# Optimization experiments

Hardware: AMD Instinct MI355X
Metric: run time of the kernel (lower is better)

## Reference

```python
import jax, jax.numpy as jnp
from jax import lax
import numpy as np

C = 56; DI = 112; DS = 16; R = 4; K = 4; NB = 10; UP = 3
B, H, W = 1, 64, 64

def conv2d(x, w, b=None, pad=1, groups=1):
    out = lax.conv_general_dilated(x, w, (1, 1), [(pad, pad), (pad, pad)],
                                   feature_group_count=groups,
                                   dimension_numbers=('NCHW', 'OIHW', 'NCHW'))
    if b is not None:
        out = out + b[None, :, None, None]
    return out

def ln_last(x, w, b, eps=1e-5):
    mu = x.mean(-1, keepdims=True)
    var = ((x - mu) ** 2).mean(-1, keepdims=True)
    return (x - mu) / jnp.sqrt(var + eps) * w + b

def ln_cf(x, w, b, eps=1e-6):
    mu = x.mean(1, keepdims=True)
    var = ((x - mu) ** 2).mean(1, keepdims=True)
    return (x - mu) / jnp.sqrt(var + eps) * w[None, :, None, None] + b[None, :, None, None]

def bsconv(x, pw_w, dw_w, dw_b):
    x = conv2d(x, pw_w, pad=0)
    return conv2d(x, dw_w, dw_b, pad=1, groups=dw_w.shape[0])

def ss2d(x, p):
    # x: (B,H,W,C) -> SS2D (VMamba 4-direction selective scan)
    b, h, w, _ = x.shape
    L = h * w
    xz = x @ p['inproj_w'].T                        # (B,H,W,2*DI)
    xin, z = jnp.split(xz, 2, axis=-1)
    xc = jnp.transpose(xin, (0, 3, 1, 2))           # (B,DI,H,W)
    xc = jax.nn.silu(conv2d(xc, p['conv_w'], p['conv_b'], pad=1, groups=DI))
    xf = xc.reshape(b, DI, L)
    xt = jnp.swapaxes(xc, 2, 3).reshape(b, DI, L)
    x_hwwh = jnp.stack([xf, xt], axis=1)            # (B,2,DI,L)
    xs = jnp.concatenate([x_hwwh, jnp.flip(x_hwwh, -1)], axis=1)  # (B,K,DI,L)
    x_dbl = jnp.einsum('bkdl,kcd->bkcl', xs, p['xproj_w'])
    dts, Bs, Cs = jnp.split(x_dbl, [R, R + DS], axis=2)
    dts = jnp.einsum('bkrl,kdr->bkdl', dts, p['dt_w'])
    A = -jnp.exp(p['Alog'].reshape(K, DI, DS))
    delta = jax.nn.softplus(dts + p['dt_b'][None, :, :, None])    # (B,K,DI,L)

    def step(hst, inp):
        dl, xl, bl, cl = inp
        dA = jnp.exp(dl[..., None] * A[None])       # (B,K,DI,DS)
        hst = dA * hst + (dl * xl)[..., None] * bl[:, :, None, :]
        y = jnp.einsum('bkdn,bkn->bkd', hst, cl)
        return hst, y

    seq = (jnp.transpose(delta, (3, 0, 1, 2)), jnp.transpose(xs, (3, 0, 1, 2)),
           jnp.transpose(Bs, (3, 0, 1, 2)), jnp.transpose(Cs, (3, 0, 1, 2)))
    h0 = jnp.zeros((b, K, DI, DS), x.dtype)
    _, ys = lax.scan(step, h0, seq)                 # (L,B,K,DI)
    out_y = jnp.transpose(ys, (1, 2, 3, 0)) + p['D'].reshape(K, DI)[None, :, :, None] * xs
    inv = jnp.flip(out_y[:, 2:4], -1)
    y1 = out_y[:, 0]
    y2 = inv[:, 0]
    y3 = jnp.swapaxes(inv[:, 1].reshape(b, DI, w, h), 2, 3).reshape(b, DI, L)
    y4 = jnp.swapaxes(out_y[:, 1].reshape(b, DI, w, h), 2, 3).reshape(b, DI, L)
    y = jnp.swapaxes(y1 + y2 + y3 + y4, 1, 2).reshape(b, h, w, DI)
    y = ln_last(y, p['onorm_w'], p['onorm_b'])
    y = y * jax.nn.silu(z)
    return y @ p['outproj_w'].T

def safm(x, mfr_w, mfr_b, aggr_w, aggr_b):
    b, c, h, w = x.shape
    ch = c // 4
    parts = jnp.split(x, 4, axis=1)
    outs = []
    for i in range(4):
        s = parts[i]
        f = 2 ** i
        if i > 0:
            s = s.reshape(b, ch, h // f, f, w // f, f).max(axis=(3, 5))
        s = conv2d(s, mfr_w[i], mfr_b[i], pad=1, groups=ch)
        if i > 0:
            s = jnp.repeat(jnp.repeat(s, f, axis=2), f, axis=3)
        outs.append(s)
    out = conv2d(jnp.concatenate(outs, axis=1), aggr_w, aggr_b, pad=0)
    return jax.nn.gelu(out, approximate=False) * x

def afd(x, p):
    xn = jnp.transpose(x, (0, 2, 3, 1))
    xn = xn + ss2d(ln_last(xn, p['ln1_w'], p['ln1_b']), p)   # VSSBlock residual
    x = jnp.transpose(xn, (0, 3, 1, 2))
    x = x + safm(ln_cf(x, p['norm_w'], p['norm_b']), p['mfr_w'], p['mfr_b'], p['aggr_w'], p['aggr_b'])
    return x, x

def _forward(x, fea_pw_w, fea_dw_w, fea_dw_b,
             blk_ln1_w, blk_ln1_b, blk_inproj_w, blk_conv_w, blk_conv_b,
             blk_xproj_w, blk_dt_w, blk_dt_b, blk_Alog, blk_D,
             blk_onorm_w, blk_onorm_b, blk_outproj_w,
             blk_norm_w, blk_norm_b, blk_mfr_w, blk_mfr_b, blk_aggr_w, blk_aggr_b,
             c1_w, c1_b, norm_w, norm_b, c2_pw_w, c2_dw_w, c2_dw_b, up_w, up_b):
    out_fea = bsconv(x, fea_pw_w, fea_dw_w, fea_dw_b)
    bp = {'ln1_w': blk_ln1_w, 'ln1_b': blk_ln1_b, 'inproj_w': blk_inproj_w,
          'conv_w': blk_conv_w, 'conv_b': blk_conv_b, 'xproj_w': blk_xproj_w,
          'dt_w': blk_dt_w, 'dt_b': blk_dt_b, 'Alog': blk_Alog, 'D': blk_D,
          'onorm_w': blk_onorm_w, 'onorm_b': blk_onorm_b, 'outproj_w': blk_outproj_w,
          'norm_w': blk_norm_w, 'norm_b': blk_norm_b, 'mfr_w': blk_mfr_w,
          'mfr_b': blk_mfr_b, 'aggr_w': blk_aggr_w, 'aggr_b': blk_aggr_b}
    _, outs = lax.scan(afd, out_fea, bp)            # (NB,B,C,H,W) in B1..B10 order
    b, _, h, w = out_fea.shape
    trunk = jnp.transpose(outs, (1, 0, 2, 3, 4)).reshape(b, NB * C, h, w)
    out_B = conv2d(trunk, c1_w, c1_b, pad=0)
    out_B = jax.nn.gelu(ln_cf(out_B, norm_w, norm_b), approximate=False)
    out_lr = bsconv(out_B, c2_pw_w, c2_dw_w, c2_dw_b) + out_fea
    up = conv2d(out_lr, up_w, up_b, pad=1)          # (B, 3*UP*UP, H, W)
    oc = up.shape[1] // (UP * UP)
    ps = up.reshape(b, oc, UP, UP, h, w)
    return jnp.transpose(ps, (0, 1, 4, 2, 5, 3)).reshape(b, oc, h * UP, w * UP)

def setup_inputs():
    key = jax.random.key(0)
    ks = iter(jax.random.split(key, 40))
    rn = lambda shape, s=0.05: jax.random.normal(next(ks), shape, jnp.float32) * s
    ones = lambda shape: jnp.ones(shape, jnp.float32)
    zeros = lambda shape: jnp.zeros(shape, jnp.float32)
    return {
        'x': jax.random.normal(next(ks), (B, 3, H, W), jnp.float32),
        'fea_pw_w': rn((C, 3, 1, 1), 0.3),
        'fea_dw_w': rn((C, 1, 3, 3), 0.3),
        'fea_dw_b': zeros((C,)),
        'blk_ln1_w': ones((NB, C)), 'blk_ln1_b': zeros((NB, C)),
        'blk_inproj_w': rn((NB, 2 * DI, C)),
        'blk_conv_w': rn((NB, DI, 1, 3, 3), 0.2), 'blk_conv_b': zeros((NB, DI)),
        'blk_xproj_w': rn((NB, K, R + 2 * DS, DI)),
        'blk_dt_w': rn((NB, K, DI, R), 0.2),
        'blk_dt_b': jnp.full((NB, K, DI), -4.6, jnp.float32),
        'blk_Alog': jnp.broadcast_to(jnp.log(jnp.arange(1, DS + 1, dtype=jnp.float32)), (NB, K * DI, DS)) + jnp.zeros((NB, K * DI, DS), jnp.float32),
        'blk_D': ones((NB, K * DI)),
        'blk_onorm_w': ones((NB, DI)), 'blk_onorm_b': zeros((NB, DI)),
        'blk_outproj_w': rn((NB, C, DI)),
        'blk_norm_w': ones((NB, C)), 'blk_norm_b': zeros((NB, C)),
        'blk_mfr_w': rn((NB, 4, C // 4, 1, 3, 3), 0.2), 'blk_mfr_b': zeros((NB, 4, C // 4)),
        'blk_aggr_w': rn((NB, C, C, 1, 1)), 'blk_aggr_b': zeros((NB, C)),
        'c1_w': rn((C, NB * C, 1, 1)), 'c1_b': zeros((C,)),
        'norm_w': ones((C,)), 'norm_b': zeros((C,)),
        'c2_pw_w': rn((C, C, 1, 1)), 'c2_dw_w': rn((C, 1, 3, 3), 0.2), 'c2_dw_b': zeros((C,)),
        'up_w': rn((3 * UP * UP, C, 3, 3)), 'up_b': zeros((3 * UP * UP,)),
    }

def reference(x, fea_pw_w, fea_dw_w, fea_dw_b,
              blk_ln1_w, blk_ln1_b, blk_inproj_w, blk_conv_w, blk_conv_b,
              blk_xproj_w, blk_dt_w, blk_dt_b, blk_Alog, blk_D,
              blk_onorm_w, blk_onorm_b, blk_outproj_w,
              blk_norm_w, blk_norm_b, blk_mfr_w, blk_mfr_b, blk_aggr_w, blk_aggr_b,
              c1_w, c1_b, norm_w, norm_b, c2_pw_w, c2_dw_w, c2_dw_b, up_w, up_b):
    return _forward(x, fea_pw_w, fea_dw_w, fea_dw_b,
                    blk_ln1_w, blk_ln1_b, blk_inproj_w, blk_conv_w, blk_conv_b,
                    blk_xproj_w, blk_dt_w, blk_dt_b, blk_Alog, blk_D,
                    blk_onorm_w, blk_onorm_b, blk_outproj_w,
                    blk_norm_w, blk_norm_b, blk_mfr_w, blk_mfr_b, blk_aggr_w, blk_aggr_b,
                    c1_w, c1_b, norm_w, norm_b, c2_pw_w, c2_dw_w, c2_dw_b, up_w, up_b)
```

## Files before the change

kernel.cpp:

```cpp
#include <hip/hip_runtime.h>
#include <hip/hip_bf16.h>

#define HW 64
#define L4 4096
#define CC 56
#define DI 112
#define DSN 16
#define NBLK 10

typedef const float* BP;

__device__ __forceinline__ float bf(BP p, int i) { return p[i]; }
__device__ __forceinline__ float siluf(float x) { return x / (1.f + __expf(-x)); }
__device__ __forceinline__ float geluf(float x) { return 0.5f * x * (1.f + erff(x * 0.70710678f)); }

__global__ void k_fea_pw(BP x, BP w, float* __restrict__ t0) {
    int tid = blockIdx.x * blockDim.x + threadIdx.x;
    if (tid >= CC * L4) return;
    int c = tid >> 12, l = tid & 4095;
    float acc = 0.f;
    for (int i = 0; i < 3; ++i) acc += bf(x, i * L4 + l) * bf(w, c * 3 + i);
    t0[tid] = acc;
}

__global__ void __launch_bounds__(256) k_dw3x3t(
        const float* __restrict__ src, BP w, BP bvec, float* __restrict__ dst,
        int act, const float* __restrict__ addsrc) {
    int c = blockIdx.x >> 4;
    int tile = blockIdx.x & 15;
    int y0 = (tile >> 2) * 16, x0 = (tile & 3) * 16;
    __shared__ float sT[18 * 18];
    const float* sc = src + (size_t)c * L4;
    for (int idx = threadIdx.x; idx < 324; idx += 256) {
        int iy = idx / 18, ix = idx - iy * 18;
        int gy = y0 - 1 + iy, gx = x0 - 1 + ix;
        sT[idx] = (gy >= 0 && gy < 64 && gx >= 0 && gx < 64) ? sc[gy * 64 + gx] : 0.f;
    }
    __syncthreads();
    int py = threadIdx.x >> 4, px = threadIdx.x & 15;
    BP wr = w + c * 9;
    float acc = bvec ? bvec[c] : 0.f;
    #pragma unroll
    for (int ky = 0; ky < 3; ++ky)
        #pragma unroll
        for (int kx = 0; kx < 3; ++kx)
            acc += sT[(py + ky) * 18 + px + kx] * wr[ky * 3 + kx];
    if (act) acc = siluf(acc);
    int l = (y0 + py) * 64 + x0 + px;
    if (addsrc) acc += addsrc[(size_t)c * L4 + l];
    dst[(size_t)c * L4 + l] = acc;
}

__global__ void __launch_bounds__(256) k_ln56(
        const float* __restrict__ src, BP w, BP b, float* __restrict__ dst,
        float eps, int gelu_after) {
    int lane = threadIdx.x & 63;
    int cg = threadIdx.x >> 6;
    int l0 = blockIdx.x * 64;
    __shared__ float sS[56 * 64];
    __shared__ float sPa[4][64], sPb[4][64];
    __shared__ float sMu[64], sRs[64];
    float ps = 0.f, ps2 = 0.f;
    for (int c = cg * 14; c < cg * 14 + 14; ++c) {
        float v = src[(size_t)c * L4 + l0 + lane];
        sS[c * 64 + lane] = v; ps += v; ps2 += v * v;
    }
    sPa[cg][lane] = ps; sPb[cg][lane] = ps2;
    __syncthreads();
    if (threadIdx.x < 64) {
        float s = sPa[0][lane] + sPa[1][lane] + sPa[2][lane] + sPa[3][lane];
        float s2 = sPb[0][lane] + sPb[1][lane] + sPb[2][lane] + sPb[3][lane];
        float mu = s / 56.f;
        float var = fmaxf(s2 / 56.f - mu * mu, 0.f);
        sMu[lane] = mu; sRs[lane] = rsqrtf(var + eps);
    }
    __syncthreads();
    float mu = sMu[lane], rs = sRs[lane];
    for (int c = cg * 14; c < cg * 14 + 14; ++c) {
        float v = (sS[c * 64 + lane] - mu) * rs * w[c] + b[c];
        if (gelu_after) v = geluf(v);
        dst[(size_t)c * L4 + l0 + lane] = v;
    }
}

__global__ void __launch_bounds__(256) k_gemm(
        const float* __restrict__ src, BP w, BP bvec, const float* __restrict__ addsrc,
        float* __restrict__ dst, int nin, int nout) {
    int lane = threadIdx.x & 63;
    int jg = threadIdx.x >> 6;
    int l0 = blockIdx.x * 64;
    int j0 = blockIdx.y * 16;
    __shared__ __align__(16) float sS[56 * 64];
    __shared__ __align__(16) float sw[16 * 56];
    float acc[4] = {0.f, 0.f, 0.f, 0.f};

    for (int i0 = 0; i0 < nin; i0 += 56) {
        __syncthreads();
        for (int idx = threadIdx.x; idx < 56 * 64; idx += 256) {
            int ii = idx >> 6, px = idx & 63;
            sS[idx] = src[(size_t)(i0 + ii) * L4 + l0 + px];
        }
        for (int idx = threadIdx.x; idx < 16 * 56; idx += 256) {
            int jj = idx / 56, ii = idx - jj * 56;
            int j = j0 + jj;
            sw[idx] = (j < nout) ? w[(size_t)j * nin + i0 + ii] : 0.f;
        }
        __syncthreads();
        #pragma unroll
        for (int ii = 0; ii < 56; ii += 4) {
            float s0 = sS[(ii + 0) * 64 + lane];
            float s1 = sS[(ii + 1) * 64 + lane];
            float s2 = sS[(ii + 2) * 64 + lane];
            float s3 = sS[(ii + 3) * 64 + lane];
            #pragma unroll
            for (int jj = 0; jj < 4; ++jj) {
                const float4 wv = *(const float4*)&sw[(jg * 4 + jj) * 56 + ii];
                acc[jj] += s0 * wv.x + s1 * wv.y + s2 * wv.z + s3 * wv.w;
            }
        }
    }
    int l = l0 + lane;
    #pragma unroll
    for (int jj = 0; jj < 4; ++jj) {
        int j = j0 + jg * 4 + jj;
        if (j >= nout) continue;
        float v = acc[jj];
        if (bvec) v += bf(bvec, j);
        size_t idx = (size_t)j * L4 + l;
        if (addsrc) v += addsrc[idx];
        dst[idx] = v;
    }
}

__global__ void __launch_bounds__(256) k_xproj(
        const float* __restrict__ src, BP w, float* __restrict__ dst) {
    int lane = threadIdx.x & 31;
    int jg = threadIdx.x >> 5;
    int l0 = blockIdx.x * 32;
    int j0 = blockIdx.y * 16;
    __shared__ __align__(16) float sS[112 * 32];
    __shared__ __align__(16) float sw[16 * 112];
    float acc[2] = {0.f, 0.f};

    for (int idx = threadIdx.x; idx < 112 * 32; idx += 256) {
        int ii = idx >> 5, px = idx & 31;
        sS[idx] = src[(size_t)ii * L4 + l0 + px];
    }
    for (int idx = threadIdx.x; idx < 16 * 112; idx += 256) {
        int jj = idx / 112, ii = idx - jj * 112;
        sw[idx] = w[(size_t)(j0 + jj) * 112 + ii];
    }
    __syncthreads();
    #pragma unroll
    for (int ii = 0; ii < 112; ii += 4) {
        float s0 = sS[(ii + 0) * 32 + lane];
        float s1 = sS[(ii + 1) * 32 + lane];
        float s2 = sS[(ii + 2) * 32 + lane];
        float s3 = sS[(ii + 3) * 32 + lane];
        #pragma unroll
        for (int jj = 0; jj < 2; ++jj) {
            const float4 wv = *(const float4*)&sw[(jg * 2 + jj) * 112 + ii];
            acc[jj] += s0 * wv.x + s1 * wv.y + s2 * wv.z + s3 * wv.w;
        }
    }
    __syncthreads();
    #pragma unroll
    for (int jj = 0; jj < 2; ++jj)
        sS[(jg * 2 + jj) * 32 + lane] = acc[jj];
    __syncthreads();
    for (int idx = threadIdx.x; idx < 16 * 32; idx += 256) {
        int cidx = idx & 15, l2 = idx >> 4;
        int j = j0 + cidx;
        int k = j / 36, c = j - k * 36;
        dst[((size_t)k * L4 + l0 + l2) * 36 + c] = sS[cidx * 32 + l2];
    }
}

__global__ void __launch_bounds__(256) k_gemm_ln(
        const float* __restrict__ src, BP lnw, BP lnb, BP w,
        float* __restrict__ dst, int nout) {
    int lane = threadIdx.x & 63;
    int jg = threadIdx.x >> 6;
    int l0 = blockIdx.x * 64;
    int j0 = blockIdx.y * 16;
    __shared__ __align__(16) float sS[56 * 64];
    __shared__ __align__(16) float sw[16 * 56];
    __shared__ float sLw[56], sLb[56];
    float acc[4] = {0.f, 0.f, 0.f, 0.f};

    for (int idx = threadIdx.x; idx < 56 * 64; idx += 256) {
        int ii = idx >> 6, px = idx & 63;
        sS[idx] = src[(size_t)ii * L4 + l0 + px];
    }
    for (int idx = threadIdx.x; idx < 16 * 56; idx += 256) {
        int jj = idx / 56, ii = idx - jj * 56;
        int j = j0 + jj;
        sw[idx] = (j < nout) ? w[(size_t)j * 56 + ii] : 0.f;
    }
    if (threadIdx.x < 56) { sLw[threadIdx.x] = lnw[threadIdx.x]; sLb[threadIdx.x] = lnb[threadIdx.x]; }
    __syncthreads();
    if (threadIdx.x < 64) {
        int px = threadIdx.x;
        float s = 0.f, s2 = 0.f;
        for (int ii = 0; ii < 56; ++ii) { float v = sS[ii * 64 + px]; s += v; s2 += v * v; }
        float mu = s / 56.f;
        float var = fmaxf(s2 / 56.f - mu * mu, 0.f);
        float rstd = rsqrtf(var + 1e-5f);
        for (int ii = 0; ii < 56; ++ii)
            sS[ii * 64 + px] = (sS[ii * 64 + px] - mu) * rstd * sLw[ii] + sLb[ii];
    }
    __syncthreads();
    #pragma unroll
    for (int ii = 0; ii < 56; ii += 4) {
        float s0 = sS[(ii + 0) * 64 + lane];
        float s1 = sS[(ii + 1) * 64 + lane];
        float s2 = sS[(ii + 2) * 64 + lane];
        float s3 = sS[(ii + 3) * 64 + lane];
        #pragma unroll
        for (int jj = 0; jj < 4; ++jj) {
            const float4 wv = *(const float4*)&sw[(jg * 4 + jj) * 56 + ii];
            acc[jj] += s0 * wv.x + s1 * wv.y + s2 * wv.z + s3 * wv.w;
        }
    }
    int l = l0 + lane;
    #pragma unroll
    for (int jj = 0; jj < 4; ++jj) {
        int j = j0 + jg * 4 + jj;
        if (j < nout) dst[(size_t)j * L4 + l] = acc[jj];
    }
}

#define SPAD(p) ((p) + ((p) >> 5))
__global__ void __launch_bounds__(1024) k_scan(
        const float* __restrict__ xc, const float* __restrict__ pk,
        BP Alog, BP dtw, BP dtb, float* __restrict__ ybuf) {
    int pair = blockIdx.x;
    int n = threadIdx.x & 15;
    int c = threadIdx.x >> 4;
    int k = pair / DI, d = pair - k * DI;
    float a = -__expf(Alog[pair * DSN + n]);
    float w0 = dtw[pair * 4 + 0], w1 = dtw[pair * 4 + 1];
    float w2 = dtw[pair * 4 + 2], w3 = dtw[pair * 4 + 3];
    float db = dtb[pair];
    const float* xptr = xc + (size_t)d * L4;
    const float* pkk = pk + (size_t)k * L4 * 36;
    float* yptr = ybuf + (size_t)pair * L4;

    __shared__ float sDl[4224];
    __shared__ float sDlx[4224];
    __shared__ float sP[64 * 16];
    __shared__ float sHe[64 * 16];
    __shared__ float sCar[64 * 16];

    for (int p = threadIdx.x; p < L4; p += 1024) {
        const float* row = pkk + (size_t)p * 36;
        float v = db + row[0] * w0 + row[1] * w1 + row[2] * w2 + row[3] * w3;
        float dl = fmaxf(v, 0.f) + __logf(1.f + __expf(-fabsf(v)));
        sDl[SPAD(p)] = dl;
        sDlx[SPAD(p)] = dl * xptr[p];
    }
    __syncthreads();

    int p0, dp;
    if (k == 0)      { p0 = c * 64;        dp = 1;   }
    else if (k == 1) { p0 = c;             dp = 64;  }
    else if (k == 2) { p0 = 4095 - c * 64; dp = -1;  }
    else             { p0 = 4095 - c;      dp = -64; }
    long rstep = (long)dp * 36;

    float h = 0.f, P = 1.f;
    {
        int p = p0;
        const float* rB = pkk + (size_t)p0 * 36 + 4 + n;
        #pragma unroll 4
        for (int j = 0; j < 64; ++j) {
            int q = SPAD(p);
            float e = __expf(sDl[q] * a);
            h = e * h + sDlx[q] * (*rB);
            P *= e;
            p += dp; rB += rstep;
        }
    }
    sP[c * 16 + n] = P;
    sHe[c * 16 + n] = h;
    __syncthreads();

    if (threadIdx.x < 16) {
        float H = 0.f;
        for (int cc = 0; cc < 64; ++cc) {
            sCar[cc * 16 + n] = H;
            H = sP[cc * 16 + n] * H + sHe[cc * 16 + n];
        }
    }
    __syncthreads();

    h = sCar[c * 16 + n];
    {
        int p = p0;
        const float* rB = pkk + (size_t)p0 * 36 + 4 + n;
        const float* rC = pkk + (size_t)p0 * 36 + 20 + n;
        #pragma unroll 4
        for (int j = 0; j < 64; ++j) {
            int q = SPAD(p);
            float e = __expf(sDl[q] * a);
            h = e * h + sDlx[q] * (*rB);
            float y = h * (*rC);
            y += __shfl_xor(y, 1, 16);
            y += __shfl_xor(y, 2, 16);
            y += __shfl_xor(y, 4, 16);
            y += __shfl_xor(y, 8, 16);
            if (n == 0) yptr[p] = y;
            p += dp; rB += rstep; rC += rstep;
        }
    }
}

__global__ void __launch_bounds__(256) k_comb_proj(
        const float* __restrict__ ybuf, const float* __restrict__ xc,
        const float* __restrict__ zbuf, BP Dp, BP ow, BP ob, BP opw,
        const float* __restrict__ xin, BP nw, BP nbv,
        float* __restrict__ x_mid, float* __restrict__ xln) {
    int lane = threadIdx.x & 63;
    int cg = threadIdx.x >> 6;
    int l0 = blockIdx.x * 64;
    __shared__ __align__(16) float sY[112 * 64];
    __shared__ __align__(16) float sW[56 * 112];
    __shared__ float sPa[4][64], sPb[4][64];
    __shared__ float sMu[64], sRs[64];

    float ps = 0.f, ps2 = 0.f;
    for (int d = cg * 28; d < cg * 28 + 28; ++d) {
        float Ds = Dp[d] + Dp[DI + d] + Dp[2 * DI + d] + Dp[3 * DI + d];
        float v = ybuf[(size_t)d * L4 + l0 + lane]
                + ybuf[(size_t)(DI + d) * L4 + l0 + lane]
                + ybuf[(size_t)(2 * DI + d) * L4 + l0 + lane]
                + ybuf[(size_t)(3 * DI + d) * L4 + l0 + lane]
                + Ds * xc[(size_t)d * L4 + l0 + lane];
        sY[d * 64 + lane] = v; ps += v; ps2 += v * v;
    }
    sPa[cg][lane] = ps; sPb[cg][lane] = ps2;
    for (int idx = threadIdx.x; idx < 56 * 112; idx += 256) sW[idx] = opw[idx];
    __syncthreads();
    if (threadIdx.x < 64) {
        float s = sPa[0][lane] + sPa[1][lane] + sPa[2][lane] + sPa[3][lane];
        float s2 = sPb[0][lane] + sPb[1][lane] + sPb[2][lane] + sPb[3][lane];
        float mu = s / 112.f;
        float var = fmaxf(s2 / 112.f - mu * mu, 0.f);
        sMu[lane] = mu; sRs[lane] = rsqrtf(var + 1e-5f);
    }
    __syncthreads();
    {
        float mu = sMu[lane], rs = sRs[lane];
        for (int d = cg * 28; d < cg * 28 + 28; ++d) {
            float v = (sY[d * 64 + lane] - mu) * rs * ow[d] + ob[d];
            float z = zbuf[(size_t)d * L4 + l0 + lane];
            sY[d * 64 + lane] = v * siluf(z);
        }
    }
    __syncthreads();

    float acc[14];
    #pragma unroll
    for (int jj = 0; jj < 14; ++jj) acc[jj] = 0.f;
    #pragma unroll 2
    for (int ii = 0; ii < 112; ii += 4) {
        float s0 = sY[(ii + 0) * 64 + lane];
        float s1 = sY[(ii + 1) * 64 + lane];
        float s2 = sY[(ii + 2) * 64 + lane];
        float s3 = sY[(ii + 3) * 64 + lane];
        #pragma unroll
        for (int jj = 0; jj < 14; ++jj) {
            const float4 wv = *(const float4*)&sW[(cg * 14 + jj) * 112 + ii];
            acc[jj] += s0 * wv.x + s1 * wv.y + s2 * wv.z + s3 * wv.w;
        }
    }
    int l = l0 + lane;
    float ps3 = 0.f, ps4 = 0.f;
    #pragma unroll
    for (int jj = 0; jj < 14; ++jj) {
        int j = cg * 14 + jj;
        float v = acc[jj] + xin[(size_t)j * L4 + l];
        acc[jj] = v;
        x_mid[(size_t)j * L4 + l] = v;
        ps3 += v; ps4 += v * v;
    }
    __syncthreads();
    sPa[cg][lane] = ps3; sPb[cg][lane] = ps4;
    __syncthreads();
    if (threadIdx.x < 64) {
        float s = sPa[0][lane] + sPa[1][lane] + sPa[2][lane] + sPa[3][lane];
        float s2 = sPb[0][lane] + sPb[1][lane] + sPb[2][lane] + sPb[3][lane];
        float mu = s / 56.f;
        float var = fmaxf(s2 / 56.f - mu * mu, 0.f);
        sMu[lane] = mu; sRs[lane] = rsqrtf(var + 1e-6f);
    }
    __syncthreads();
    {
        float mu = sMu[lane], rs = sRs[lane];
        #pragma unroll
        for (int jj = 0; jj < 14; ++jj) {
            int j = cg * 14 + jj;
            xln[(size_t)j * L4 + l] = (acc[jj] - mu) * rs * nw[j] + nbv[j];
        }
    }
}

__global__ void __launch_bounds__(256) k_safm(
        const float* __restrict__ xln, BP mw, BP mb,
        float* __restrict__ s0, float* __restrict__ s1,
        float* __restrict__ s2, float* __restrict__ s3) {
    int b = blockIdx.x;
    if (b < 224) {
        int c = b >> 4;
        int tile = b & 15;
        int y0 = (tile >> 2) * 16, x0 = (tile & 3) * 16;
        __shared__ float sT[18 * 18];
        const float* sc = xln + (size_t)c * L4;
        for (int idx = threadIdx.x; idx < 324; idx += 256) {
            int iy = idx / 18, ix = idx - iy * 18;
            int gy = y0 - 1 + iy, gx = x0 - 1 + ix;
            sT[idx] = (gy >= 0 && gy < 64 && gx >= 0 && gx < 64) ? sc[gy * 64 + gx] : 0.f;
        }
        __syncthreads();
        int py = threadIdx.x >> 4, px = threadIdx.x & 15;
        BP wr = mw + c * 9;
        float acc = mb[c];
        #pragma unroll
        for (int ky = 0; ky < 3; ++ky)
            #pragma unroll
            for (int kx = 0; kx < 3; ++kx)
                acc += sT[(py + ky) * 18 + px + kx] * wr[ky * 3 + kx];
        s0[c * L4 + (y0 + py) * 64 + x0 + px] = acc;
    } else {
        int bb = b - 224;
        int i = bb / 14 + 1;
        int c = bb % 14;
        int S = 64 >> i;
        int f = 1 << i;
        __shared__ float sP[34 * 34];
        int W2 = S + 2;
        for (int idx = threadIdx.x; idx < W2 * W2; idx += 256) sP[idx] = 0.f;
        __syncthreads();
        const float* sc = xln + (size_t)(i * 14 + c) * L4;
        for (int cell = threadIdx.x; cell < S * S; cell += 256) {
            int y = cell / S, x = cell - y * S;
            float m = -3.4e38f;
            for (int dy = 0; dy < f; ++dy)
                for (int dx = 0; dx < f; ++dx)
                    m = fmaxf(m, sc[(y * f + dy) * 64 + x * f + dx]);
            sP[(y + 1) * W2 + x + 1] = m;
        }
        __syncthreads();
        BP wr = mw + (i * 14 + c) * 9;
        float bias = mb[i * 14 + c];
        float* dst = (i == 1) ? s1 : (i == 2) ? s2 : s3;
        for (int cell = threadIdx.x; cell < S * S; cell += 256) {
            int y = cell / S, x = cell - y * S;
            float acc = bias;
            #pragma unroll
            for (int ky = 0; ky < 3; ++ky)
                #pragma unroll
                for (int kx = 0; kx < 3; ++kx)
                    acc += sP[(y + ky) * W2 + x + kx] * wr[ky * 3 + kx];
            dst[c * S * S + cell] = acc;
        }
    }
}

__global__ void k_aggr(const float* __restrict__ s0, const float* __restrict__ s1,
                       const float* __restrict__ s2, const float* __restrict__ s3,
                       const float* __restrict__ xln, const float* __restrict__ x_mid,
                       BP aw, BP ab, float* __restrict__ out) {
    int tid = blockIdx.x * blockDim.x + threadIdx.x;
    if (tid >= CC * L4) return;
    int c = tid >> 12, l = tid & 4095;
    int h = l >> 6, w = l & 63;
    int o1 = (h >> 1) * 32 + (w >> 1);
    int o2 = (h >> 2) * 16 + (w >> 2);
    int o3 = (h >> 3) * 8 + (w >> 3);
    float acc = bf(ab, c);
    BP wr = aw + c * 56;
    for (int cg = 0; cg < 14; ++cg) acc += s0[cg * 4096 + l]  * bf(wr, cg);
    for (int cg = 0; cg < 14; ++cg) acc += s1[cg * 1024 + o1] * bf(wr, 14 + cg);
    for (int cg = 0; cg < 14; ++cg) acc += s2[cg * 256 + o2]  * bf(wr, 28 + cg);
    for (int cg = 0; cg < 14; ++cg) acc += s3[cg * 64 + o3]   * bf(wr, 42 + cg);
    out[tid] = x_mid[tid] + geluf(acc) * xln[tid];
}

__global__ void __launch_bounds__(256) k_up(
        const float* __restrict__ out_lr, BP uw, BP ub, float* __restrict__ out) {
    __shared__ float sIn[56 * 36];
    __shared__ float sW[27 * 56 * 9];
    int b = blockIdx.x;
    int y0 = (b >> 4) * 4, x0 = (b & 15) * 4;
    for (int idx = threadIdx.x; idx < 56 * 36; idx += 256) {
        int cc = idx / 36; int rem = idx - cc * 36; int iy = rem / 6, ix = rem - iy * 6;
        int gy = y0 - 1 + iy, gx = x0 - 1 + ix;
        sIn[idx] = (gy >= 0 && gy < 64 && gx >= 0 && gx < 64)
                 ? out_lr[(size_t)cc * L4 + gy * 64 + gx] : 0.f;
    }
    for (int idx = threadIdx.x; idx < 27 * 56 * 9; idx += 256) sW[idx] = uw[idx];
    __syncthreads();
    int px = threadIdx.x & 15;
    int og = threadIdx.x >> 4;
    int dy = px >> 2, dx = px & 3;
    for (int oo = 0; oo < 2; ++oo) {
        int o = og * 2 + oo;
        if (o >= 27) break;
        float acc = ub[o];
        const float* wb = &sW[o * 504];
        for (int cc = 0; cc < 56; ++cc) {
            const float* ib = &sIn[cc * 36 + dy * 6 + dx];
            const float* wc = wb + cc * 9;
            acc += ib[0] * wc[0] + ib[1] * wc[1] + ib[2] * wc[2]
                 + ib[6] * wc[3] + ib[7] * wc[4] + ib[8] * wc[5]
                 + ib[12] * wc[6] + ib[13] * wc[7] + ib[14] * wc[8];
        }
        int h = y0 + dy, wv = x0 + dx;
        int ch = o / 9, rr = (o % 9) / 3, ss = o % 3;
        out[ch * 36864 + (h * 3 + rr) * 192 + (wv * 3 + ss)] = acc;
    }
}

extern "C" void kernel_launch(void* const* d_in, const int* in_sizes, int n_in,
                              void* d_out, int out_size, void* d_ws, size_t ws_size,
                              hipStream_t stream) {
    BP in0  = (BP)d_in[0];
    BP in1  = (BP)d_in[1];
    BP in2  = (BP)d_in[2];
    BP in3  = (BP)d_in[3];
    BP in4  = (BP)d_in[4];
    BP in5  = (BP)d_in[5];
    BP in6  = (BP)d_in[6];
    BP in7  = (BP)d_in[7];
    BP in8  = (BP)d_in[8];
    BP in9  = (BP)d_in[9];
    BP in10 = (BP)d_in[10];
    BP in11 = (BP)d_in[11];
    BP in12 = (BP)d_in[12];
    BP in13 = (BP)d_in[13];
    BP in14 = (BP)d_in[14];
    BP in15 = (BP)d_in[15];
    BP in16 = (BP)d_in[16];
    BP in17 = (BP)d_in[17];
    BP in18 = (BP)d_in[18];
    BP in19 = (BP)d_in[19];
    BP in20 = (BP)d_in[20];
    BP in21 = (BP)d_in[21];
    BP in22 = (BP)d_in[22];
    BP in23 = (BP)d_in[23];
    BP in24 = (BP)d_in[24];
    BP in25 = (BP)d_in[25];
    BP in26 = (BP)d_in[26];
    BP in27 = (BP)d_in[27];
    BP in28 = (BP)d_in[28];
    BP in29 = (BP)d_in[29];
    BP in30 = (BP)d_in[30];
    BP in31 = (BP)d_in[31];

    float* ws = (float*)d_ws;
    float* trunk   = ws; ws += 560 * L4;
    float* out_fea = ws; ws += CC * L4;
    float* t0      = ws; ws += CC * L4;
    float* xz      = ws; ws += 224 * L4;
    float* xc      = ws; ws += DI * L4;
    float* pk      = ws; ws += 4 * 36 * L4;
    float* ybuf    = ws; ws += 4 * DI * L4;
    float* x_mid   = ws; ws += CC * L4;
    float* xln     = ws; ws += CC * L4;
    float* s0      = ws; ws += 14 * 4096;
    float* s1      = ws; ws += 14 * 1024;
    float* s2      = ws; ws += 14 * 256;
    float* s3      = ws; ws += 14 * 64;
    float* bufB    = ws; ws += CC * L4;
    float* gB      = ws; ws += CC * L4;
    float* tbuf    = ws; ws += CC * L4;
    float* out_lr  = ws; ws += CC * L4;

    auto nb256 = [](int n) { return dim3((n + 255) / 256); };
    auto gemm_grid = [](int nout) { return dim3(64, (nout + 15) / 16); };

    k_fea_pw<<<nb256(CC * L4), 256, 0, stream>>>(in0, in1, t0);
    k_dw3x3t<<<dim3(CC * 16), 256, 0, stream>>>(t0, in2, in3, out_fea, 0, nullptr);

    for (int nb = 0; nb < NBLK; ++nb) {
        const float* xin = (nb == 0) ? out_fea : trunk + (size_t)(nb - 1) * CC * L4;
        float* xout = trunk + (size_t)nb * CC * L4;
        BP ln1w = in4 + nb * 56,        ln1b = in5 + nb * 56;
        BP ipw  = in6 + nb * 224 * 56;
        BP cw   = in7 + nb * 112 * 9,   cb   = in8 + nb * 112;
        BP xpw  = in9 + nb * 4 * 36 * 112;
        BP dtw  = in10 + nb * 4 * 112 * 4, dtb = in11 + nb * 448;
        BP alog = in12 + nb * 448 * 16, Dp   = in13 + nb * 448;
        BP onw  = in14 + nb * 112,      onb  = in15 + nb * 112;
        BP opw  = in16 + nb * 56 * 112;
        BP nw   = in17 + nb * 56,       nbv  = in18 + nb * 56;
        BP mw   = in19 + nb * 4 * 14 * 9, mb = in20 + nb * 56;
        BP aw   = in21 + nb * 56 * 56,  ab   = in22 + nb * 56;

        k_gemm_ln<<<gemm_grid(224), 256, 0, stream>>>(xin, ln1w, ln1b, ipw, xz, 224);
        k_dw3x3t<<<dim3(DI * 16), 256, 0, stream>>>(xz, cw, cb, xc, 1, nullptr);
        k_xproj<<<dim3(128, 9), 256, 0, stream>>>(xc, xpw, pk);
        k_scan<<<dim3(4 * DI), 1024, 0, stream>>>(xc, pk, alog, dtw, dtb, ybuf);
        k_comb_proj<<<dim3(64), 256, 0, stream>>>(ybuf, xc, xz + 112 * L4, Dp, onw, onb, opw,
                                                  xin, nw, nbv, x_mid, xln);
        k_safm<<<dim3(266), 256, 0, stream>>>(xln, mw, mb, s0, s1, s2, s3);
        k_aggr<<<nb256(CC * L4), 256, 0, stream>>>(s0, s1, s2, s3, xln, x_mid, aw, ab, xout);
    }

    k_gemm<<<gemm_grid(56), 256, 0, stream>>>(trunk, in23, in24, nullptr, bufB, 560, 56);
    k_ln56<<<dim3(64), 256, 0, stream>>>(bufB, in25, in26, gB, 1e-6f, 1);
    k_gemm<<<gemm_grid(56), 256, 0, stream>>>(gB, in27, nullptr, nullptr, tbuf, 56, 56);
    k_dw3x3t<<<dim3(CC * 16), 256, 0, stream>>>(tbuf, in28, in29, out_lr, 0, out_fea);
    k_up<<<dim3(256), 256, 0, stream>>>(out_lr, in30, in31, (float*)d_out);
}
```

Baseline: 1.407 ms.

## Split-K the final 1x1 conv, parallelize scan carry, and shrink comb_proj tiles

The final 560-input 1x1 conv is split along K into 5 slices, each writing partial sums. A new LN kernel adds the partials and the bias before normalizing and applying GELU. The serial 64-step carry propagation in the scan kernel becomes a log-step Hillis-Steele prefix over chunks. k_comb_proj moves from 64 blocks of 64 pixels to 256 blocks of 16 pixels to raise occupancy. In exchange, the partials cost extra memory traffic, the prefix scan adds more block syncs, and each comb_proj block now reloads the full weight matrix.

```diff
diff --git a/kernel.cpp b/kernel.cpp
--- a/kernel.cpp
+++ b/kernel.cpp
@@ -51,9 +51,8 @@
     dst[(size_t)c * L4 + l] = acc;
 }
 
-__global__ void __launch_bounds__(256) k_ln56(
-        const float* __restrict__ src, BP w, BP b, float* __restrict__ dst,
-        float eps, int gelu_after) {
+__global__ void __launch_bounds__(256) k_ln56g(
+        const float* __restrict__ part, BP bias, BP w, BP b, float* __restrict__ dst) {
     int lane = threadIdx.x & 63;
     int cg = threadIdx.x >> 6;
     int l0 = blockIdx.x * 64;
@@ -62,7 +61,10 @@
     __shared__ float sMu[64], sRs[64];
     float ps = 0.f, ps2 = 0.f;
     for (int c = cg * 14; c < cg * 14 + 14; ++c) {
-        float v = src[(size_t)c * L4 + l0 + lane];
+        float v = bias[c];
+        #pragma unroll
+        for (int z = 0; z < 5; ++z)
+            v += part[(size_t)(z * 56 + c) * L4 + l0 + lane];
         sS[c * 64 + lane] = v; ps += v; ps2 += v * v;
     }
     sPa[cg][lane] = ps; sPb[cg][lane] = ps2;
@@ -72,14 +74,13 @@
         float s2 = sPb[0][lane] + sPb[1][lane] + sPb[2][lane] + sPb[3][lane];
         float mu = s / 56.f;
         float var = fmaxf(s2 / 56.f - mu * mu, 0.f);
-        sMu[lane] = mu; sRs[lane] = rsqrtf(var + eps);
+        sMu[lane] = mu; sRs[lane] = rsqrtf(var + 1e-6f);
     }
     __syncthreads();
     float mu = sMu[lane], rs = sRs[lane];
     for (int c = cg * 14; c < cg * 14 + 14; ++c) {
         float v = (sS[c * 64 + lane] - mu) * rs * w[c] + b[c];
-        if (gelu_after) v = geluf(v);
-        dst[(size_t)c * L4 + l0 + lane] = v;
+        dst[(size_t)c * L4 + l0 + lane] = geluf(v);
     }
 }
 
@@ -129,6 +130,50 @@
         size_t idx = (size_t)j * L4 + l;
         if (addsrc) v += addsrc[idx];
         dst[idx] = v;
+    }
+}
+
+__global__ void __launch_bounds__(256) k_c1(
+        const float* __restrict__ src, BP w, float* __restrict__ part) {
+    int lane = threadIdx.x & 63;
+    int jg = threadIdx.x >> 6;
+    int l0 = blockIdx.x * 64;
+    int j0 = blockIdx.y * 16;
+    int z = blockIdx.z;
+    __shared__ __align__(16) float sS[56 * 64];
+    __shared__ __align__(16) float sw[16 * 56];
+    float acc[4] = {0.f, 0.f, 0.f, 0.f};
+
+    for (int i0 = z * 112; i0 < z * 112 + 112; i0 += 56) {
+        __syncthreads();
+        for (int idx = threadIdx.x; idx < 56 * 64; idx += 256) {
+            int ii = idx >> 6, px = idx & 63;
+            sS[idx] = src[(size_t)(i0 + ii) * L4 + l0 + px];
+        }
+        for (int idx = threadIdx.x; idx < 16 * 56; idx += 256) {
+            int jj = idx / 56, ii = idx - jj * 56;
+            int j = j0 + jj;
+            sw[idx] = (j < 56) ? w[(size_t)j * 560 + i0 + ii] : 0.f;
+        }
+        __syncthreads();
+        #pragma unroll
+        for (int ii = 0; ii < 56; ii += 4) {
+            float s0 = sS[(ii + 0) * 64 + lane];
+            float s1 = sS[(ii + 1) * 64 + lane];
+            float s2 = sS[(ii + 2) * 64 + lane];
+            float s3 = sS[(ii + 3) * 64 + lane];
+            #pragma unroll
+            for (int jj = 0; jj < 4; ++jj) {
+                const float4 wv = *(const float4*)&sw[(jg * 4 + jj) * 56 + ii];
+                acc[jj] += s0 * wv.x + s1 * wv.y + s2 * wv.z + s3 * wv.w;
+            }
+        }
+    }
+    int l = l0 + lane;
+    #pragma unroll
+    for (int jj = 0; jj < 4; ++jj) {
+        int j = j0 + jg * 4 + jj;
+        if (j < 56) part[(size_t)(z * 56 + j) * L4 + l] = acc[jj];
     }
 }
 
@@ -250,7 +295,6 @@
     __shared__ float sDlx[4224];
     __shared__ float sP[64 * 16];
     __shared__ float sHe[64 * 16];
-    __shared__ float sCar[64 * 16];
 
     for (int p = threadIdx.x; p < L4; p += 1024) {
         const float* row = pkk + (size_t)p * 36;
@@ -281,20 +325,21 @@
             p += dp; rB += rstep;
         }
     }
-    sP[c * 16 + n] = P;
-    sHe[c * 16 + n] = h;
-    __syncthreads();
-
-    if (threadIdx.x < 16) {
-        float H = 0.f;
-        for (int cc = 0; cc < 64; ++cc) {
-            sCar[cc * 16 + n] = H;
-            H = sP[cc * 16 + n] * H + sHe[cc * 16 + n];
-        }
-    }
-    __syncthreads();
-
-    h = sCar[c * 16 + n];
+    int idx = c * 16 + n;
+    sP[idx] = P;
+    sHe[idx] = h;
+    __syncthreads();
+
+    for (int off = 1; off < 64; off <<= 1) {
+        float pC = sP[idx], hC = sHe[idx];
+        float pL = 0.f, hL = 0.f;
+        if (c >= off) { pL = sP[idx - off * 16]; hL = sHe[idx - off * 16]; }
+        __syncthreads();
+        if (c >= off) { sP[idx] = pC * pL; sHe[idx] = pC * hL + hC; }
+        __syncthreads();
+    }
+
+    h = (c > 0) ? sHe[idx - 16] : 0.f;
     {
         int p = p0;
         const float* rB = pkk + (size_t)p0 * 36 + 4 + n;
@@ -320,30 +365,30 @@
         const float* __restrict__ zbuf, BP Dp, BP ow, BP ob, BP opw,
         const float* __restrict__ xin, BP nw, BP nbv,
         float* __restrict__ x_mid, float* __restrict__ xln) {
-    int lane = threadIdx.x & 63;
-    int cg = threadIdx.x >> 6;
-    int l0 = blockIdx.x * 64;
-    __shared__ __align__(16) float sY[112 * 64];
+    int lane = threadIdx.x & 15;
+    int grp = threadIdx.x >> 4;
+    int l0 = blockIdx.x * 16;
+    __shared__ __align__(16) float sY[112 * 16];
     __shared__ __align__(16) float sW[56 * 112];
-    __shared__ float sPa[4][64], sPb[4][64];
-    __shared__ float sMu[64], sRs[64];
+    __shared__ float sPa[16][16], sPb[16][16];
+    __shared__ float sMu[16], sRs[16];
 
     float ps = 0.f, ps2 = 0.f;
-    for (int d = cg * 28; d < cg * 28 + 28; ++d) {
+    for (int d = grp * 7; d < grp * 7 + 7; ++d) {
         float Ds = Dp[d] + Dp[DI + d] + Dp[2 * DI + d] + Dp[3 * DI + d];
         float v = ybuf[(size_t)d * L4 + l0 + lane]
                 + ybuf[(size_t)(DI + d) * L4 + l0 + lane]
                 + ybuf[(size_t)(2 * DI + d) * L4 + l0 + lane]
                 + ybuf[(size_t)(3 * DI + d) * L4 + l0 + lane]
                 + Ds * xc[(size_t)d * L4 + l0 + lane];
-        sY[d * 64 + lane] = v; ps += v; ps2 += v * v;
-    }
-    sPa[cg][lane] = ps; sPb[cg][lane] = ps2;
+        sY[d * 16 + lane] = v; ps += v; ps2 += v * v;
+    }
+    sPa[grp][lane] = ps; sPb[grp][lane] = ps2;
     for (int idx = threadIdx.x; idx < 56 * 112; idx += 256) sW[idx] = opw[idx];
     __syncthreads();
-    if (threadIdx.x < 64) {
-        float s = sPa[0][lane] + sPa[1][lane] + sPa[2][lane] + sPa[3][lane];
-        float s2 = sPb[0][lane] + sPb[1][lane] + sPb[2][lane] + sPb[3][lane];
+    if (threadIdx.x < 16) {
+        float s = 0.f, s2 = 0.f;
+        for (int g = 0; g < 16; ++g) { s += sPa[g][lane]; s2 += sPb[g][lane]; }
         float mu = s / 112.f;
         float var = fmaxf(s2 / 112.f - mu * mu, 0.f);
         sMu[lane] = mu; sRs[lane] = rsqrtf(var + 1e-5f);
@@ -351,45 +396,50 @@
     __syncthreads();
     {
         float mu = sMu[lane], rs = sRs[lane];
-        for (int d = cg * 28; d < cg * 28 + 28; ++d) {
-            float v = (sY[d * 64 + lane] - mu) * rs * ow[d] + ob[d];
+        for (int d = grp * 7; d < grp * 7 + 7; ++d) {
+            float v = (sY[d * 16 + lane] - mu) * rs * ow[d] + ob[d];
             float z = zbuf[(size_t)d * L4 + l0 + lane];
-            sY[d * 64 + lane] = v * siluf(z);
-        }
-    }
-    __syncthreads();
-
-    float acc[14];
-    #pragma unroll
-    for (int jj = 0; jj < 14; ++jj) acc[jj] = 0.f;
+            sY[d * 16 + lane] = v * siluf(z);
+        }
+    }
+    __syncthreads();
+
+    float acc[4] = {0.f, 0.f, 0.f, 0.f};
     #pragma unroll 2
     for (int ii = 0; ii < 112; ii += 4) {
-        float s0 = sY[(ii + 0) * 64 + lane];
-        float s1 = sY[(ii + 1) * 64 + lane];
-        float s2 = sY[(ii + 2) * 64 + lane];
-        float s3 = sY[(ii + 3) * 64 + lane];
-        #pragma unroll
-        for (int jj = 0; jj < 14; ++jj) {
-            const float4 wv = *(const float4*)&sW[(cg * 14 + jj) * 112 + ii];
-            acc[jj] += s0 * wv.x + s1 * wv.y + s2 * wv.z + s3 * wv.w;
+        float s0 = sY[(ii + 0) * 16 + lane];
+        float s1 = sY[(ii + 1) * 16 + lane];
+        float s2 = sY[(ii + 2) * 16 + lane];
+        float s3 = sY[(ii + 3) * 16 + lane];
+        #pragma unroll
+        for (int jj = 0; jj < 4; ++jj) {
+            int j = grp * 4 + jj;
+            if (j < 56) {
+                const float4 wv = *(const float4*)&sW[j * 112 + ii];
+                acc[jj] += s0 * wv.x + s1 * wv.y + s2 * wv.z + s3 * wv.w;
+            }
         }
     }
     int l = l0 + lane;
+    float vout[4];
     float ps3 = 0.f, ps4 = 0.f;
     #pragma unroll
-    for (int jj = 0; jj < 14; ++jj) {
-        int j = cg * 14 + jj;
-        float v = acc[jj] + xin[(size_t)j * L4 + l];
-        acc[jj] = v;
-        x_mid[(size_t)j * L4 + l] = v;
-        ps3 += v; ps4 += v * v;
-    }
-    __syncthreads();
-    sPa[cg][lane] = ps3; sPb[cg][lane] = ps4;
-    __syncthreads();
-    if (threadIdx.x < 64) {
-        float s = sPa[0][lane] + sPa[1][lane] + sPa[2][lane] + sPa[3][lane];
-        float s2 = sPb[0][lane] + sPb[1][lane] + sPb[2][lane] + sPb[3][lane];
+    for (int jj = 0; jj < 4; ++jj) {
+        int j = grp * 4 + jj;
+        vout[jj] = 0.f;
+        if (j < 56) {
+            float v = acc[jj] + xin[(size_t)j * L4 + l];
+            vout[jj] = v;
+            x_mid[(size_t)j * L4 + l] = v;
+            ps3 += v; ps4 += v * v;
+        }
+    }
+    __syncthreads();
+    sPa[grp][lane] = ps3; sPb[grp][lane] = ps4;
+    __syncthreads();
+    if (threadIdx.x < 16) {
+        float s = 0.f, s2 = 0.f;
+        for (int g = 0; g < 16; ++g) { s += sPa[g][lane]; s2 += sPb[g][lane]; }
         float mu = s / 56.f;
         float var = fmaxf(s2 / 56.f - mu * mu, 0.f);
         sMu[lane] = mu; sRs[lane] = rsqrtf(var + 1e-6f);
@@ -398,9 +448,9 @@
     {
         float mu = sMu[lane], rs = sRs[lane];
         #pragma unroll
-        for (int jj = 0; jj < 14; ++jj) {
-            int j = cg * 14 + jj;
-            xln[(size_t)j * L4 + l] = (acc[jj] - mu) * rs * nw[j] + nbv[j];
+        for (int jj = 0; jj < 4; ++jj) {
+            int j = grp * 4 + jj;
+            if (j < 56) xln[(size_t)j * L4 + l] = (vout[jj] - mu) * rs * nw[j] + nbv[j];
         }
     }
 }
@@ -572,7 +622,7 @@
     float* s1      = ws; ws += 14 * 1024;
     float* s2      = ws; ws += 14 * 256;
     float* s3      = ws; ws += 14 * 64;
-    float* bufB    = ws; ws += CC * L4;
+    float* part    = ws; ws += 5 * 56 * L4;
     float* gB      = ws; ws += CC * L4;
     float* tbuf    = ws; ws += CC * L4;
     float* out_lr  = ws; ws += CC * L4;
@@ -602,14 +652,14 @@
         k_dw3x3t<<<dim3(DI * 16), 256, 0, stream>>>(xz, cw, cb, xc, 1, nullptr);
         k_xproj<<<dim3(128, 9), 256, 0, stream>>>(xc, xpw, pk);
         k_scan<<<dim3(4 * DI), 1024, 0, stream>>>(xc, pk, alog, dtw, dtb, ybuf);
-        k_comb_proj<<<dim3(64), 256, 0, stream>>>(ybuf, xc, xz + 112 * L4, Dp, onw, onb, opw,
-                                                  xin, nw, nbv, x_mid, xln);
+        k_comb_proj<<<dim3(256), 256, 0, stream>>>(ybuf, xc, xz + 112 * L4, Dp, onw, onb, opw,
+                                                   xin, nw, nbv, x_mid, xln);
         k_safm<<<dim3(266), 256, 0, stream>>>(xln, mw, mb, s0, s1, s2, s3);
         k_aggr<<<nb256(CC * L4), 256, 0, stream>>>(s0, s1, s2, s3, xln, x_mid, aw, ab, xout);
     }
 
-    k_gemm<<<gemm_grid(56), 256, 0, stream>>>(trunk, in23, in24, nullptr, bufB, 560, 56);
-    k_ln56<<<dim3(64), 256, 0, stream>>>(bufB, in25, in26, gB, 1e-6f, 1);
+    k_c1<<<dim3(64, 4, 5), 256, 0, stream>>>(trunk, in23, part);
+    k_ln56g<<<dim3(64), 256, 0, stream>>>(part, in24, in25, in26, gB);
     k_gemm<<<gemm_grid(56), 256, 0, stream>>>(gB, in27, nullptr, nullptr, tbuf, 56, 56);
     k_dw3x3t<<<dim3(CC * 16), 256, 0, stream>>>(tbuf, in28, in29, out_lr, 0, out_fea);
     k_up<<<dim3(256), 256, 0, stream>>>(out_lr, in30, in31, (float*)d_out);
```

New measurement: 1.300 ms. -7.7%, faster.
